# Kernel tuning notes

Measured on AMD Instinct MI355X. Metric: run time of the kernel, lower is better.

## Reference

```python
import jax, jax.numpy as jnp
import numpy as np
from jax import lax


def _mdlstm_dir(x, Wx, Wh, Wv, b):
    # x: [H, W, B, Cin]; one diagonal-causal 2D-LSTM scan (top-left origin).
    H, W, B, Cin = x.shape
    C = Wh.shape[0]
    xa = jnp.einsum('hwbi,ic->hwbc', x, Wx) + b  # [H,W,B,5C] precomputed input gates

    def col_step(carry, inp):
        h_l, c_l = carry                    # left neighbor [B,C]
        xa_ij, h_u, c_u = inp               # input preact, up neighbor
        a = xa_ij + h_l @ Wh + h_u @ Wv     # [B,5C]
        i, f1, f2, o, g = jnp.split(a, 5, axis=-1)
        c = jax.nn.sigmoid(i) * jnp.tanh(g) + jax.nn.sigmoid(f1) * c_l + jax.nn.sigmoid(f2) * c_u
        h = jax.nn.sigmoid(o) * jnp.tanh(c)
        return (h, c), (h, c)

    z = jnp.zeros((B, C), x.dtype)
    zrow = jnp.zeros((W, B, C), x.dtype)

    def row_step(carry, xa_row):
        h_up, c_up = carry                  # [W,B,C]
        _, (hs, cs) = lax.scan(col_step, (z, z), (xa_row, h_up, c_up))
        return (hs, cs), hs

    _, hh = lax.scan(row_step, (zrow, zrow), xa)  # [H,W,B,C]
    return hh


def _mdlstm4(x, Wx, Wh, Wv, b):
    # x: [B,Cin,H,W] -> per-direction outputs [4,H,W,B,C] (directions: TL, TR, BL, BR origins)
    xt = jnp.transpose(x, (2, 3, 0, 1))  # [H,W,B,Cin]
    x4 = jnp.stack([xt, xt[:, ::-1], xt[::-1], xt[::-1, ::-1]])
    o = jax.vmap(_mdlstm_dir)(x4, Wx, Wh, Wv, b)  # [4,H,W,B,C]
    return jnp.stack([o[0], o[1][:, ::-1], o[2][::-1], o[3][::-1, ::-1]])


def _block(x, Wx, Wh, Wv, b, cw, cb):
    h4 = _mdlstm4(x, Wx, Wh, Wv, b)            # [4,H,W,B,C]
    h = jnp.transpose(h4.sum(0), (2, 3, 0, 1))  # sum directions -> [B,C,H,W]
    y = lax.conv_general_dilated(h, cw, window_strides=(2, 2), padding='VALID',
                                 dimension_numbers=('NCHW', 'OIHW', 'NCHW'))
    return jnp.tanh(y + cb[None, :, None, None])


def _forward(x, p0_Wx, p0_Wh, p0_Wv, p0_b, c0_w, c0_b,
             p1_Wx, p1_Wh, p1_Wv, p1_b, c1_w, c1_b,
             p2_Wx, p2_Wh, p2_Wv, p2_b, dW, db):
    x = _block(x, p0_Wx, p0_Wh, p0_Wv, p0_b, c0_w, c0_b)  # [B,6,31,126]
    x = _block(x, p1_Wx, p1_Wh, p1_Wv, p1_b, c1_w, c1_b)  # [B,20,14,61]
    h4 = _mdlstm4(x, p2_Wx, p2_Wh, p2_Wv, p2_b)           # [4,H,W,B,50]
    # per-direction Linear(50->100) then sum over the 4 directions
    out = jnp.einsum('dhwbc,dcn->bhwn', h4, dW) + db.sum(0)
    return out  # [B,14,61,100]


def setup_inputs() -> dict:
    key = jax.random.key(0)
    ks = jax.random.split(key, 20)
    rn = lambda k, s, sc=0.1: jax.random.normal(k, s, jnp.float32) * sc
    return {
        'x': jax.random.normal(ks[0], (16, 1, 64, 256), jnp.float32),
        'p0_Wx': rn(ks[1], (4, 1, 10)), 'p0_Wh': rn(ks[2], (4, 2, 10)),
        'p0_Wv': rn(ks[3], (4, 2, 10)), 'p0_b': rn(ks[4], (4, 10)),
        'c0_w': rn(ks[5], (6, 2, 2, 4)), 'c0_b': rn(ks[6], (6,)),
        'p1_Wx': rn(ks[7], (4, 6, 50)), 'p1_Wh': rn(ks[8], (4, 10, 50)),
        'p1_Wv': rn(ks[9], (4, 10, 50)), 'p1_b': rn(ks[10], (4, 50)),
        'c1_w': rn(ks[11], (20, 10, 2, 4)), 'c1_b': rn(ks[12], (20,)),
        'p2_Wx': rn(ks[13], (4, 20, 250)), 'p2_Wh': rn(ks[14], (4, 50, 250)),
        'p2_Wv': rn(ks[15], (4, 50, 250)), 'p2_b': rn(ks[16], (4, 250)),
        'dW': rn(ks[17], (4, 50, 100)), 'db': rn(ks[18], (4, 100)),
    }


def reference(x, p0_Wx, p0_Wh, p0_Wv, p0_b, c0_w, c0_b,
              p1_Wx, p1_Wh, p1_Wv, p1_b, c1_w, c1_b,
              p2_Wx, p2_Wh, p2_Wv, p2_b, dW, db):
    return _forward(x, p0_Wx, p0_Wh, p0_Wv, p0_b, c0_w, c0_b,
                    p1_Wx, p1_Wh, p1_Wv, p1_b, c1_w, c1_b,
                    p2_Wx, p2_Wh, p2_Wv, p2_b, dW, db)
```

## Files before the change

### kernel.cpp

```cpp
#include <hip/hip_runtime.h>

typedef unsigned short ushort_t;
typedef __attribute__((ext_vector_type(8))) short short8;
typedef __attribute__((ext_vector_type(4))) float float4_t;
typedef __attribute__((ext_vector_type(2))) float v2f;

__device__ __forceinline__ float frcp(float x) { return __builtin_amdgcn_rcpf(x); }
__device__ __forceinline__ float fsig(float x) { return frcp(1.f + __expf(-x)); }
__device__ __forceinline__ float ftanh(float x) { return 1.f - 2.f * frcp(1.f + __expf(2.f * x)); }
__device__ __forceinline__ float sig_e2(float a) { return frcp(1.f + __builtin_amdgcn_exp2f(a)); }
__device__ __forceinline__ float th_e2(float a) { return 1.f - 2.f * frcp(1.f + __builtin_amdgcn_exp2f(a)); }

__device__ __forceinline__ ushort_t f2bf(float f) {
    union { float f; unsigned u; } v; v.f = f;
    unsigned u = v.u;
    unsigned r = (u + 0x7fffu + ((u >> 16) & 1u)) >> 16;
    return (ushort_t)r;
}
__device__ __forceinline__ float bf2f(ushort_t s) {
    union { unsigned u; float f; } v; v.u = ((unsigned)s) << 16;
    return v.f;
}
__device__ __forceinline__ float dpp_shr1(float x) {
    int i = __builtin_bit_cast(int, x);
    int r = __builtin_amdgcn_update_dpp(0, i, 0x138 , 0xf, 0xf, true);
    return __builtin_bit_cast(float, r);
}

__global__ __launch_bounds__(64) void k_mdlstm0(
    const float* __restrict__ x, const float* __restrict__ Wx,
    const float* __restrict__ Wh, const float* __restrict__ Wv,
    const float* __restrict__ bias, float* __restrict__ h0)
{
    const int dir = blockIdx.x >> 4, b = blockIdx.x & 15;
    const int lane = threadIdx.x;
    const bool fH = dir >= 2, fW = (dir & 1) != 0;
    const int ri = fH ? 63 - lane : lane;
    const float L2E = 1.44269504088896340736f;

    __shared__ float Xs[64 * 256];
    {
        const float* xg = x + b * 64 * 256;
        for (int i4 = lane; i4 < 4096; i4 += 64) {
            int row = i4 >> 6, c4 = (i4 & 63) << 2;
            float4 v = *(const float4*)(xg + (row << 8) + c4);
            *(float4*)&Xs[(row << 8) + c4] = v;
        }
    }
    __syncthreads();

    v2f wx[5], bs[5], wh0[5], wh1[5], wv0[5], wv1[5];
#pragma unroll
    for (int g = 0; g < 5; g++) {
        float sc = (g == 4) ? 2.f * L2E : -L2E;
#pragma unroll
        for (int un = 0; un < 2; un++) {
            int n = g * 2 + un;
            wx[g][un]  = Wx[dir * 10 + n] * sc;
            bs[g][un]  = bias[dir * 10 + n] * sc;
            wh0[g][un] = Wh[(dir * 2 + 0) * 10 + n] * sc;
            wh1[g][un] = Wh[(dir * 2 + 1) * 10 + n] * sc;
            wv0[g][un] = Wv[(dir * 2 + 0) * 10 + n] * sc;
            wv1[g][un] = Wv[(dir * 2 + 1) * 10 + n] * sc;
        }
    }

    float* orow = h0 + (((dir * 16 + b) * 64 + ri) * 256) * 2;
    v2f hr = {0.f, 0.f}, cr = {0.f, 0.f};

    auto ld = [&](int d) -> float {
        int j = d - lane; j = j < 0 ? 0 : (j > 255 ? 255 : j);
        int cj = fW ? 255 - j : j;
        return Xs[(ri << 8) + cj];
    };
    float xp0 = ld(0), xp1 = ld(1);

    for (int d = 0; d < 319; d++) {
        float xv = xp0;
        xp0 = xp1;
        xp1 = ld(d + 2);

        float hu0 = dpp_shr1(hr.x), hu1 = dpp_shr1(hr.y);
        float cu0 = dpp_shr1(cr.x), cu1 = dpp_shr1(cr.y);

        int j = d - lane;
        if (j >= 0 && j < 256) {
            v2f a[5];
#pragma unroll
            for (int g = 0; g < 5; g++) {
                v2f t = __builtin_elementwise_fma((v2f){xv, xv}, wx[g], bs[g]);
                t = __builtin_elementwise_fma((v2f){hr.x, hr.x}, wh0[g], t);
                t = __builtin_elementwise_fma((v2f){hr.y, hr.y}, wh1[g], t);
                t = __builtin_elementwise_fma((v2f){hu0, hu0}, wv0[g], t);
                t = __builtin_elementwise_fma((v2f){hu1, hu1}, wv1[g], t);
                a[g] = t;
            }
            v2f si  = {sig_e2(a[0].x), sig_e2(a[0].y)};
            v2f sf1 = {sig_e2(a[1].x), sig_e2(a[1].y)};
            v2f sf2 = {sig_e2(a[2].x), sig_e2(a[2].y)};
            v2f so  = {sig_e2(a[3].x), sig_e2(a[3].y)};
            v2f tg  = {th_e2(a[4].x),  th_e2(a[4].y)};
            v2f cu  = {cu0, cu1};
            v2f cn = si * tg + sf1 * cr + sf2 * cu;
            v2f tc = {th_e2(cn.x * (2.f * L2E)), th_e2(cn.y * (2.f * L2E))};
            hr = so * tc;
            cr = cn;
            int cj = fW ? 255 - j : j;
            float2 hv; hv.x = hr.x; hv.y = hr.y;
            *(float2*)&orow[cj * 2] = hv;
        } else {
            hr = (v2f){0.f, 0.f};
            cr = (v2f){0.f, 0.f};
        }
    }
}

__global__ __launch_bounds__(128) void k_conv0(
    const float* __restrict__ h0, const float* __restrict__ cw,
    const float* __restrict__ cb, float* __restrict__ x1)
{
    int blk = blockIdx.x;
    int oh = blk / 127, ow = blk % 127;
    int t = threadIdx.x;
    if (t >= 96) return;
    int b = t / 6, co = t % 6;
    float w[2][2][4];
#pragma unroll
    for (int ci = 0; ci < 2; ci++)
#pragma unroll
        for (int kh = 0; kh < 2; kh++)
#pragma unroll
            for (int kw = 0; kw < 4; kw++)
                w[ci][kh][kw] = cw[((co * 2 + ci) * 2 + kh) * 4 + kw];
    float acc = cb[co];
    for (int dirb = 0; dirb < 4; dirb++) {
#pragma unroll
        for (int kh = 0; kh < 2; kh++) {
#pragma unroll
            for (int kw = 0; kw < 4; kw++) {
                const float* ptr = h0 + ((((dirb * 16 + b) * 64) + (2 * oh + kh)) * 256 + (2 * ow + kw)) * 2;
                float2 hv = *(const float2*)ptr;
                acc = fmaf(hv.x, w[0][kh][kw], acc);
                acc = fmaf(hv.y, w[1][kh][kw], acc);
            }
        }
    }
    x1[((oh * 127 + ow) * 16 + b) * 6 + co] = ftanh(acc);
}

__global__ __launch_bounds__(1024, 1) void k_mdlstm1(
    const float* __restrict__ x1, const float* __restrict__ Wx,
    const float* __restrict__ Wh, const float* __restrict__ Wv,
    const float* __restrict__ bias, float* __restrict__ h1)
{
    const int dir = blockIdx.x >> 4, b = blockIdx.x & 15;
    const bool fH = dir >= 2, fW = (dir & 1) != 0;
    const int tid = threadIdx.x;
    const int wave = tid >> 6, lane = tid & 63;

    __shared__ float Xs1[32 * 127 * 6];
    __shared__ __align__(16) ushort_t Ah[2][32][40];
    __shared__ __align__(16) ushort_t Al[2][32][40];
    __shared__ float P[32][68];
    __shared__ float cbuf[2][33][12];

    for (int i = tid; i < 2 * 32 * 40; i += 1024) { ((ushort_t*)Ah)[i] = 0; ((ushort_t*)Al)[i] = 0; }
    for (int i = tid; i < 2 * 33 * 12; i += 1024) ((float*)cbuf)[i] = 0.f;
    for (int i = tid; i < 32 * 127 * 6; i += 1024)
        Xs1[i] = x1[(i / 6) * 96 + b * 6 + (i % 6)];
    __syncthreads();
    if (tid < 6) {
        int rr = fH ? 31 : 0, cc = fW ? 126 : 0;
        float xv = Xs1[(rr * 127 + cc) * 6 + tid];
        ushort_t xh = f2bf(xv);
        Ah[0][0][20 + tid] = xh;
        Al[0][0][20 + tid] = f2bf(xv - bf2f(xh));
    }

    const int mt = wave & 1, nt = wave >> 1;
    short8 bh = {0,0,0,0,0,0,0,0}, bl = {0,0,0,0,0,0,0,0};
    if (wave < 8) {
        int n = nt * 16 + (lane & 15);
#pragma unroll
        for (int jj = 0; jj < 8; jj++) {
            int k = (lane >> 4) * 8 + jj;
            float v = 0.f;
            if (n < 50) {
                if (k < 10)      v = Wh[(dir * 10 + k) * 50 + n];
                else if (k < 20) v = Wv[(dir * 10 + (k - 10)) * 50 + n];
                else if (k < 26) v = Wx[(dir * 6 + (k - 20)) * 50 + n];
            }
            ushort_t hi = f2bf(v);
            bh[jj] = (short)hi;
            bl[jj] = (short)f2bf(v - bf2f(hi));
        }
    }

    const int cell = tid / 10, u = tid % 10;
    float br[5];
#pragma unroll
    for (int g = 0; g < 5; g++) br[g] = (tid < 320) ? bias[dir * 50 + g * 10 + u] : 0.f;
    const int ri = fH ? 31 - cell : cell;
    float creg = 0.f;
    __syncthreads();

    int p = 0;
    for (int d = 0; d < 158; d++) {
        if (wave < 8) {
            const int arow = mt * 16 + (lane & 15);
            const int koff = (lane >> 4) * 8;
            short8 ah = *(const short8*)&Ah[p][arow][koff];
            short8 al = *(const short8*)&Al[p][arow][koff];
            float4_t acc = {0.f, 0.f, 0.f, 0.f};
            acc = __builtin_amdgcn_mfma_f32_16x16x32_bf16(ah, bh, acc, 0, 0, 0);
            acc = __builtin_amdgcn_mfma_f32_16x16x32_bf16(al, bh, acc, 0, 0, 0);
            acc = __builtin_amdgcn_mfma_f32_16x16x32_bf16(ah, bl, acc, 0, 0, 0);
            int col = nt * 16 + (lane & 15);
            int r0 = (lane >> 4) * 4;
#pragma unroll
            for (int r = 0; r < 4; r++) P[mt * 16 + r0 + r][col] = acc[r];
        } else if (tid >= 512 && tid < 704) {
            int s = tid - 512, xc = s / 6, ci = s % 6;
            int jn = d + 1 - xc;
            if (jn >= 0 && jn < 127) {
                int rr = fH ? 31 - xc : xc, cc = fW ? 126 - jn : jn;
                float xv = Xs1[(rr * 127 + cc) * 6 + ci];
                ushort_t xh = f2bf(xv);
                Ah[1 - p][xc][20 + ci] = xh;
                Al[1 - p][xc][20 + ci] = f2bf(xv - bf2f(xh));
            }
        }
        __syncthreads();

        if (tid < 320) {
            int j = d - cell;
            if (j >= 0 && j < 127) {
                float ai  = P[cell][u]      + br[0];
                float af1 = P[cell][10 + u] + br[1];
                float af2 = P[cell][20 + u] + br[2];
                float ao  = P[cell][30 + u] + br[3];
                float ag  = P[cell][40 + u] + br[4];
                float cu = cbuf[p][cell][u];
                float cn = fsig(ai) * ftanh(ag) + fsig(af1) * creg + fsig(af2) * cu;
                float hn = fsig(ao) * ftanh(cn);
                creg = cn;
                cbuf[1 - p][cell + 1][u] = cn;
                ushort_t hh = f2bf(hn);
                float hhf = bf2f(hh);
                ushort_t hlo = f2bf(hn - hhf);
                Ah[1 - p][cell][u] = hh;
                Al[1 - p][cell][u] = hlo;
                if (cell < 31) { Ah[1 - p][cell + 1][10 + u] = hh; Al[1 - p][cell + 1][10 + u] = hlo; }
                int cj = fW ? 126 - j : j;
                h1[(((dir * 16 + b) * 32 + ri) * 127 + cj) * 10 + u] = hn;
            }
        }
        __syncthreads();
        p ^= 1;
    }
}

__global__ __launch_bounds__(320, 1) void k_conv1(
    const float* __restrict__ h1, const float* __restrict__ cw,
    const float* __restrict__ cb, float* __restrict__ x2)
{
    int blk = blockIdx.x;
    int oh = blk / 62, ow = blk % 62;
    int t = threadIdx.x;
    int b = t / 20, co = t % 20;
    float w[10][2][4];
#pragma unroll
    for (int ci = 0; ci < 10; ci++)
#pragma unroll
        for (int kh = 0; kh < 2; kh++)
#pragma unroll
            for (int kw = 0; kw < 4; kw++)
                w[ci][kh][kw] = cw[((co * 10 + ci) * 2 + kh) * 4 + kw];
    float acc = cb[co];
    for (int dirb = 0; dirb < 4; dirb++) {
#pragma unroll
        for (int kh = 0; kh < 2; kh++) {
#pragma unroll
            for (int kw = 0; kw < 4; kw++) {
                const float* ptr = h1 + ((((dirb * 16 + b) * 32) + (2 * oh + kh)) * 127 + (2 * ow + kw)) * 10;
#pragma unroll
                for (int ci = 0; ci < 10; ci++)
                    acc = fmaf(ptr[ci], w[ci][kh][kw], acc);
            }
        }
    }
    x2[((oh * 62 + ow) * 16 + b) * 20 + co] = ftanh(acc);
}

__global__ __launch_bounds__(256) void k_prepB2(
    const float* __restrict__ Wh, const float* __restrict__ Wv,
    const float* __restrict__ Wx, ushort_t* __restrict__ Bh,
    ushort_t* __restrict__ Bl)
{
    int idx = blockIdx.x * 256 + threadIdx.x;
    if (idx >= 131072) return;
    int dir = idx >> 15; int k = (idx >> 8) & 127; int n = idx & 255;
    float v = 0.f;
    if (n < 250) {
        if (k < 50)       v = Wh[(dir * 50 + k) * 250 + n];
        else if (k < 100) v = Wv[(dir * 50 + (k - 50)) * 250 + n];
        else if (k < 120) v = Wx[(dir * 20 + (k - 100)) * 250 + n];
    }
    ushort_t hi = f2bf(v);
    Bh[idx] = hi;
    Bl[idx] = f2bf(v - bf2f(hi));
}

__global__ __launch_bounds__(1024, 1) void k_mdlstm2(
    const float* __restrict__ x2, const ushort_t* __restrict__ BmH,
    const ushort_t* __restrict__ BmL,
    const float* __restrict__ bias, float* __restrict__ h2)
{
    const int dir = blockIdx.x >> 4, b = blockIdx.x & 15;
    const bool fH = dir >= 2, fW = (dir & 1) != 0;
    const int tid = threadIdx.x;
    const int wave = tid >> 6, lane = tid & 63;

    __shared__ float Xs2[16 * 62 * 20];
    __shared__ __align__(16) ushort_t Ah[2][16][136];
    __shared__ __align__(16) ushort_t Al[2][16][136];
    __shared__ float P[16][260];
    __shared__ float cbuf[2][16][52];

    for (int i = tid; i < 2 * 16 * 136; i += 1024) { ((ushort_t*)Ah)[i] = 0; ((ushort_t*)Al)[i] = 0; }
    for (int i = tid; i < 16 * 62 * 20; i += 1024)
        Xs2[i] = x2[(i / 20) * 320 + b * 20 + (i % 20)];
    __syncthreads();
    if (tid < 20) {
        int ci = tid;
        int rr = fH ? 15 : 0, cc = fW ? 61 : 0;
        float xv = Xs2[(rr * 62 + cc) * 20 + ci];
        ushort_t xh = f2bf(xv);
        Ah[0][0][100 + ci] = xh;
        Al[0][0][100 + ci] = f2bf(xv - bf2f(xh));
    }

    short8 bfragH[4], bfragL[4];
    {
        const int n = wave * 16 + (lane & 15);
#pragma unroll
        for (int q = 0; q < 4; q++) {
#pragma unroll
            for (int jj = 0; jj < 8; jj++) {
                int k = q * 32 + (lane >> 4) * 8 + jj;
                bfragH[q][jj] = (short)BmH[(dir * 128 + k) * 256 + n];
                bfragL[q][jj] = (short)BmL[(dir * 128 + k) * 256 + n];
            }
        }
    }

    const int cell = tid / 50, u = tid % 50;
    float bi = 0, bf1 = 0, bf2v = 0, bo = 0, bg = 0;
    if (tid < 800) {
        bi   = bias[dir * 250 + u];
        bf1  = bias[dir * 250 + 50 + u];
        bf2v = bias[dir * 250 + 100 + u];
        bo   = bias[dir * 250 + 150 + u];
        bg   = bias[dir * 250 + 200 + u];
    }
    const int rr_c = fH ? 15 - cell : cell;
    float creg = 0.f;
    __syncthreads();

    int p = 0;
    for (int d = 0; d < 77; d++) {
        {
            const int arow = lane & 15;
            const int koff = (lane >> 4) * 8;
            short8 ah[4], al[4];
#pragma unroll
            for (int q = 0; q < 4; q++) {
                ah[q] = *(const short8*)&Ah[p][arow][q * 32 + koff];
                al[q] = *(const short8*)&Al[p][arow][q * 32 + koff];
            }
            float4_t acc = {0.f, 0.f, 0.f, 0.f};
#pragma unroll
            for (int q = 0; q < 4; q++) acc = __builtin_amdgcn_mfma_f32_16x16x32_bf16(ah[q], bfragH[q], acc, 0, 0, 0);
#pragma unroll
            for (int q = 0; q < 4; q++) acc = __builtin_amdgcn_mfma_f32_16x16x32_bf16(al[q], bfragH[q], acc, 0, 0, 0);
#pragma unroll
            for (int q = 0; q < 4; q++) acc = __builtin_amdgcn_mfma_f32_16x16x32_bf16(ah[q], bfragL[q], acc, 0, 0, 0);
            int col = wave * 16 + (lane & 15);
            int r0 = (lane >> 4) * 4;
#pragma unroll
            for (int r = 0; r < 4; r++) P[r0 + r][col] = acc[r];
        }
        __syncthreads();

        if (tid < 800) {
            int j = d - cell;
            if (j >= 0 && j < 62) {
                float ai  = P[cell][u] + bi;
                float af1 = P[cell][50 + u] + bf1;
                float af2 = P[cell][100 + u] + bf2v;
                float ao  = P[cell][150 + u] + bo;
                float ag  = P[cell][200 + u] + bg;
                float cu = (cell == 0) ? 0.f : cbuf[p][cell - 1][u];
                float cn = fsig(ai) * ftanh(ag) + fsig(af1) * creg + fsig(af2) * cu;
                float hn = fsig(ao) * ftanh(cn);
                creg = cn;
                cbuf[1 - p][cell][u] = cn;
                ushort_t hh = f2bf(hn);
                float hhf = bf2f(hh);
                ushort_t hlo = f2bf(hn - hhf);
                Ah[1 - p][cell][u] = hh;
                Al[1 - p][cell][u] = hlo;
                if (cell < 15) { Ah[1 - p][cell + 1][50 + u] = hh; Al[1 - p][cell + 1][50 + u] = hlo; }
                int cc = fW ? 61 - j : j;
                h2[(((dir * 16 + b) * 16 + rr_c) * 62 + cc) * 50 + u] = hn;
            }
        } else if (tid >= 832 && tid < 992) {
            int s = tid - 832;
#pragma unroll
            for (int it = 0; it < 2; it++) {
                int item = s + it * 160;
                int xc = item / 20, ci = item % 20;
                int jn = d + 1 - xc;
                if (jn >= 0 && jn < 62) {
                    int rr = fH ? 15 - xc : xc, cc = fW ? 61 - jn : jn;
                    float xv = Xs2[(rr * 62 + cc) * 20 + ci];
                    ushort_t xh = f2bf(xv);
                    Ah[1 - p][xc][100 + ci] = xh;
                    Al[1 - p][xc][100 + ci] = f2bf(xv - bf2f(xh));
                }
            }
        }
        __syncthreads();
        p ^= 1;
    }
}

__global__ __launch_bounds__(256) void k_final(
    const float* __restrict__ h2, const float* __restrict__ dW,
    const float* __restrict__ db, float* __restrict__ out)
{
    int blk = blockIdx.x;
    int r = blk / 62, c = blk % 62;
    int t = threadIdx.x;
    __shared__ float hb[3200];
    for (int i = t; i < 3200; i += 256) {
        int dirb = i / 800, rem = i % 800, b = rem / 50, u = rem % 50;
        hb[i] = h2[(((dirb * 16 + b) * 16 + r) * 62 + c) * 50 + u];
    }
    __syncthreads();
    for (int o = t; o < 1600; o += 256) {
        int b = o / 100, n = o % 100;
        float acc = db[n] + db[100 + n] + db[200 + n] + db[300 + n];
#pragma unroll
        for (int dirb = 0; dirb < 4; dirb++) {
            const float* hp = hb + (dirb * 16 + b) * 50;
            const float* wp = dW + dirb * 5000 + n;
#pragma unroll 10
            for (int cc2 = 0; cc2 < 50; cc2++)
                acc = fmaf(hp[cc2], wp[cc2 * 100], acc);
        }
        out[((b * 16 + r) * 62 + c) * 100 + n] = acc;
    }
}

extern "C" void kernel_launch(void* const* d_in, const int* in_sizes, int n_in,
                              void* d_out, int out_size, void* d_ws, size_t ws_size,
                              hipStream_t stream)
{
    const float* x     = (const float*)d_in[0];
    const float* p0_Wx = (const float*)d_in[1];
    const float* p0_Wh = (const float*)d_in[2];
    const float* p0_Wv = (const float*)d_in[3];
    const float* p0_b  = (const float*)d_in[4];
    const float* c0_w  = (const float*)d_in[5];
    const float* c0_b  = (const float*)d_in[6];
    const float* p1_Wx = (const float*)d_in[7];
    const float* p1_Wh = (const float*)d_in[8];
    const float* p1_Wv = (const float*)d_in[9];
    const float* p1_b  = (const float*)d_in[10];
    const float* c1_w  = (const float*)d_in[11];
    const float* c1_b  = (const float*)d_in[12];
    const float* p2_Wx = (const float*)d_in[13];
    const float* p2_Wh = (const float*)d_in[14];
    const float* p2_Wv = (const float*)d_in[15];
    const float* p2_b  = (const float*)d_in[16];
    const float* dW    = (const float*)d_in[17];
    const float* db    = (const float*)d_in[18];
    float* out = (float*)d_out;
    float* ws  = (float*)d_ws;

    float* h0 = ws;
    float* x1 = h0 + 2097152;
    float* h1 = x1 + 390144;
    float* x2 = h1 + 2600960;
    float* h2 = x2 + 317440;
    ushort_t* BmH = (ushort_t*)(h2 + 3174400);
    ushort_t* BmL = BmH + 131072;

    k_prepB2<<<512, 256, 0, stream>>>(p2_Wh, p2_Wv, p2_Wx, BmH, BmL);
    k_mdlstm0<<<64, 64, 0, stream>>>(x, p0_Wx, p0_Wh, p0_Wv, p0_b, h0);
    k_conv0<<<32 * 127, 128, 0, stream>>>(h0, c0_w, c0_b, x1);
    k_mdlstm1<<<64, 1024, 0, stream>>>(x1, p1_Wx, p1_Wh, p1_Wv, p1_b, h1);
    k_conv1<<<16 * 62, 320, 0, stream>>>(h1, c1_w, c1_b, x2);
    k_mdlstm2<<<64, 1024, 0, stream>>>(x2, BmH, BmL, p2_b, h2);
    k_final<<<16 * 62, 256, 0, stream>>>(h2, dW, db, out);
}
```

Before: 477.3 us.

## Interleave gates per unit in layer-2 MFMA tiles and fuse LSTM update; unroll layer-0 diagonal

```diff
diff --git a/kernel.cpp b/kernel.cpp
--- a/kernel.cpp
+++ b/kernel.cpp
@@ -66,51 +66,69 @@
     }
 
     float* orow = h0 + (((dir * 16 + b) * 64 + ri) * 256) * 2;
-    v2f hr = {0.f, 0.f}, cr = {0.f, 0.f};
-
-    auto ld = [&](int d) -> float {
-        int j = d - lane; j = j < 0 ? 0 : (j > 255 ? 255 : j);
-        int cj = fW ? 255 - j : j;
+    v2f hB = {0.f, 0.f}, cB = {0.f, 0.f};
+
+    auto ldx = [&](int j) -> float {
+        int jc = j < 0 ? 0 : (j > 255 ? 255 : j);
+        int cj = fW ? 255 - jc : jc;
         return Xs[(ri << 8) + cj];
     };
-    float xp0 = ld(0), xp1 = ld(1);
-
-    for (int d = 0; d < 319; d++) {
-        float xv = xp0;
-        xp0 = xp1;
-        xp1 = ld(d + 2);
-
-        float hu0 = dpp_shr1(hr.x), hu1 = dpp_shr1(hr.y);
-        float cu0 = dpp_shr1(cr.x), cu1 = dpp_shr1(cr.y);
-
-        int j = d - lane;
-        if (j >= 0 && j < 256) {
-            v2f a[5];
-#pragma unroll
-            for (int g = 0; g < 5; g++) {
-                v2f t = __builtin_elementwise_fma((v2f){xv, xv}, wx[g], bs[g]);
-                t = __builtin_elementwise_fma((v2f){hr.x, hr.x}, wh0[g], t);
-                t = __builtin_elementwise_fma((v2f){hr.y, hr.y}, wh1[g], t);
-                t = __builtin_elementwise_fma((v2f){hu0, hu0}, wv0[g], t);
-                t = __builtin_elementwise_fma((v2f){hu1, hu1}, wv1[g], t);
-                a[g] = t;
-            }
-            v2f si  = {sig_e2(a[0].x), sig_e2(a[0].y)};
-            v2f sf1 = {sig_e2(a[1].x), sig_e2(a[1].y)};
-            v2f sf2 = {sig_e2(a[2].x), sig_e2(a[2].y)};
-            v2f so  = {sig_e2(a[3].x), sig_e2(a[3].y)};
-            v2f tg  = {th_e2(a[4].x),  th_e2(a[4].y)};
-            v2f cu  = {cu0, cu1};
-            v2f cn = si * tg + sf1 * cr + sf2 * cu;
-            v2f tc = {th_e2(cn.x * (2.f * L2E)), th_e2(cn.y * (2.f * L2E))};
-            hr = so * tc;
-            cr = cn;
-            int cj = fW ? 255 - j : j;
-            float2 hv; hv.x = hr.x; hv.y = hr.y;
+    auto cellf = [&](float xv, v2f hl, v2f cl, float hu0, float hu1,
+                     float cu0, float cu1, v2f& hn, v2f& cn) {
+        v2f a[5];
+#pragma unroll
+        for (int g = 0; g < 5; g++) {
+            v2f t = __builtin_elementwise_fma((v2f){xv, xv}, wx[g], bs[g]);
+            t = __builtin_elementwise_fma((v2f){hl.x, hl.x}, wh0[g], t);
+            t = __builtin_elementwise_fma((v2f){hl.y, hl.y}, wh1[g], t);
+            t = __builtin_elementwise_fma((v2f){hu0, hu0}, wv0[g], t);
+            t = __builtin_elementwise_fma((v2f){hu1, hu1}, wv1[g], t);
+            a[g] = t;
+        }
+        v2f si  = {sig_e2(a[0].x), sig_e2(a[0].y)};
+        v2f sf1 = {sig_e2(a[1].x), sig_e2(a[1].y)};
+        v2f sf2 = {sig_e2(a[2].x), sig_e2(a[2].y)};
+        v2f so  = {sig_e2(a[3].x), sig_e2(a[3].y)};
+        v2f tg  = {th_e2(a[4].x),  th_e2(a[4].y)};
+        v2f cu  = {cu0, cu1};
+        cn = si * tg + sf1 * cl + sf2 * cu;
+        v2f tc = {th_e2(cn.x * (2.f * L2E)), th_e2(cn.y * (2.f * L2E))};
+        hn = so * tc;
+    };
+
+    float xA0 = ldx(0 - lane), xB0 = ldx(1 - lane);
+    float xA1 = ldx(2 - lane), xB1 = ldx(3 - lane);
+
+    for (int t = 0; t < 160; t++) {
+        const int jA = 2 * t - lane, jB = jA + 1;
+        float xA = xA0, xB = xB0;
+        xA0 = xA1; xB0 = xB1;
+        xA1 = ldx(2 * (t + 2) - lane); xB1 = ldx(2 * (t + 2) + 1 - lane);
+
+        float huA0 = dpp_shr1(hB.x), huA1 = dpp_shr1(hB.y);
+        float cuA0 = dpp_shr1(cB.x), cuA1 = dpp_shr1(cB.y);
+        v2f hA, cA;
+        cellf(xA, hB, cB, huA0, huA1, cuA0, cuA1, hA, cA);
+        bool actA = (jA >= 0) && (jA < 256);
+        if (!actA) { hA = (v2f){0.f, 0.f}; cA = (v2f){0.f, 0.f}; }
+
+        float huB0 = dpp_shr1(hA.x), huB1 = dpp_shr1(hA.y);
+        float cuB0 = dpp_shr1(cA.x), cuB1 = dpp_shr1(cA.y);
+        v2f hN, cN;
+        cellf(xB, hA, cA, huB0, huB1, cuB0, cuB1, hN, cN);
+        bool actB = (jB >= 0) && (jB < 256);
+        if (!actB) { hN = (v2f){0.f, 0.f}; cN = (v2f){0.f, 0.f}; }
+        hB = hN; cB = cN;
+
+        if (actA) {
+            int cj = fW ? 255 - jA : jA;
+            float2 hv; hv.x = hA.x; hv.y = hA.y;
             *(float2*)&orow[cj * 2] = hv;
-        } else {
-            hr = (v2f){0.f, 0.f};
-            cr = (v2f){0.f, 0.f};
+        }
+        if (actB) {
+            int cj = fW ? 255 - jB : jB;
+            float2 hv; hv.x = hB.x; hv.y = hB.y;
+            *(float2*)&orow[cj * 2] = hv;
         }
     }
 }
@@ -298,10 +316,15 @@
     ushort_t* __restrict__ Bl)
 {
     int idx = blockIdx.x * 256 + threadIdx.x;
-    if (idx >= 131072) return;
-    int dir = idx >> 15; int k = (idx >> 8) & 127; int n = idx & 255;
+    if (idx >= 262144) return;
+    int jj = idx & 7, lane = (idx >> 3) & 63, q = (idx >> 9) & 3;
+    int nt = (idx >> 11) & 31, dir = idx >> 16;
+    int k = q * 32 + (lane >> 4) * 8 + jj;
+    int col = nt * 16 + (lane & 15);
+    int unit = col >> 3, gate = col & 7;
     float v = 0.f;
-    if (n < 250) {
+    if (unit < 50 && gate < 5) {
+        int n = gate * 50 + unit;
         if (k < 50)       v = Wh[(dir * 50 + k) * 250 + n];
         else if (k < 100) v = Wv[(dir * 50 + (k - 50)) * 250 + n];
         else if (k < 120) v = Wx[(dir * 20 + (k - 100)) * 250 + n];
@@ -312,121 +335,131 @@
 }
 
 __global__ __launch_bounds__(1024, 1) void k_mdlstm2(
-    const float* __restrict__ x2, const ushort_t* __restrict__ BmH,
-    const ushort_t* __restrict__ BmL,
+    const float* __restrict__ x2, const ushort_t* __restrict__ BfH,
+    const ushort_t* __restrict__ BfL,
     const float* __restrict__ bias, float* __restrict__ h2)
 {
     const int dir = blockIdx.x >> 4, b = blockIdx.x & 15;
     const bool fH = dir >= 2, fW = (dir & 1) != 0;
     const int tid = threadIdx.x;
     const int wave = tid >> 6, lane = tid & 63;
+    const int quad = lane >> 4, g_self = lane & 7, uloc = (lane >> 3) & 1;
+    const float L2E = 1.44269504088896340736f;
 
     __shared__ float Xs2[16 * 62 * 20];
     __shared__ __align__(16) ushort_t Ah[2][16][136];
     __shared__ __align__(16) ushort_t Al[2][16][136];
-    __shared__ float P[16][260];
-    __shared__ float cbuf[2][16][52];
 
     for (int i = tid; i < 2 * 16 * 136; i += 1024) { ((ushort_t*)Ah)[i] = 0; ((ushort_t*)Al)[i] = 0; }
     for (int i = tid; i < 16 * 62 * 20; i += 1024)
         Xs2[i] = x2[(i / 20) * 320 + b * 20 + (i % 20)];
     __syncthreads();
     if (tid < 20) {
-        int ci = tid;
         int rr = fH ? 15 : 0, cc = fW ? 61 : 0;
-        float xv = Xs2[(rr * 62 + cc) * 20 + ci];
+        float xv = Xs2[(rr * 62 + cc) * 20 + tid];
         ushort_t xh = f2bf(xv);
-        Ah[0][0][100 + ci] = xh;
-        Al[0][0][100 + ci] = f2bf(xv - bf2f(xh));
-    }
-
-    short8 bfragH[4], bfragL[4];
-    {
-        const int n = wave * 16 + (lane & 15);
-#pragma unroll
-        for (int q = 0; q < 4; q++) {
-#pragma unroll
-            for (int jj = 0; jj < 8; jj++) {
-                int k = q * 32 + (lane >> 4) * 8 + jj;
-                bfragH[q][jj] = (short)BmH[(dir * 128 + k) * 256 + n];
-                bfragL[q][jj] = (short)BmL[(dir * 128 + k) * 256 + n];
-            }
-        }
-    }
-
-    const int cell = tid / 50, u = tid % 50;
-    float bi = 0, bf1 = 0, bf2v = 0, bo = 0, bg = 0;
-    if (tid < 800) {
-        bi   = bias[dir * 250 + u];
-        bf1  = bias[dir * 250 + 50 + u];
-        bf2v = bias[dir * 250 + 100 + u];
-        bo   = bias[dir * 250 + 150 + u];
-        bg   = bias[dir * 250 + 200 + u];
-    }
-    const int rr_c = fH ? 15 - cell : cell;
-    float creg = 0.f;
+        Ah[0][0][100 + tid] = xh;
+        Al[0][0][100 + tid] = f2bf(xv - bf2f(xh));
+    }
+
+    const bool mwave = wave < 13;
+    const float s_c = (g_self == 4) ? 2.f * L2E : -L2E;
+    const float a_c = (g_self == 4) ? -2.f : 1.f;
+    const float c_c = (g_self == 4) ? 1.f : 0.f;
+
+    int unitr[2];
+    float biasr[2];
+#pragma unroll
+    for (int t = 0; t < 2; t++) {
+        int nt = 2 * wave + t;
+        int un = 2 * nt + uloc;
+        unitr[t] = un;
+        biasr[t] = (mwave && un < 50 && g_self < 5) ? bias[dir * 250 + g_self * 50 + un] : 0.f;
+    }
+    const ushort_t* pBh = BfH + (size_t)(dir * 32 + 2 * wave) * 2048 + lane * 8;
+    const ushort_t* pBl = BfL + (size_t)(dir * 32 + 2 * wave) * 2048 + lane * 8;
+
+    float cprev[2][4] = {{0.f, 0.f, 0.f, 0.f}, {0.f, 0.f, 0.f, 0.f}};
     __syncthreads();
 
     int p = 0;
     for (int d = 0; d < 77; d++) {
-        {
+        if (mwave) {
+            float4_t acc0 = {0.f, 0.f, 0.f, 0.f}, acc1 = {0.f, 0.f, 0.f, 0.f};
             const int arow = lane & 15;
             const int koff = (lane >> 4) * 8;
-            short8 ah[4], al[4];
 #pragma unroll
             for (int q = 0; q < 4; q++) {
-                ah[q] = *(const short8*)&Ah[p][arow][q * 32 + koff];
-                al[q] = *(const short8*)&Al[p][arow][q * 32 + koff];
-            }
-            float4_t acc = {0.f, 0.f, 0.f, 0.f};
-#pragma unroll
-            for (int q = 0; q < 4; q++) acc = __builtin_amdgcn_mfma_f32_16x16x32_bf16(ah[q], bfragH[q], acc, 0, 0, 0);
-#pragma unroll
-            for (int q = 0; q < 4; q++) acc = __builtin_amdgcn_mfma_f32_16x16x32_bf16(al[q], bfragH[q], acc, 0, 0, 0);
-#pragma unroll
-            for (int q = 0; q < 4; q++) acc = __builtin_amdgcn_mfma_f32_16x16x32_bf16(ah[q], bfragL[q], acc, 0, 0, 0);
-            int col = wave * 16 + (lane & 15);
-            int r0 = (lane >> 4) * 4;
-#pragma unroll
-            for (int r = 0; r < 4; r++) P[r0 + r][col] = acc[r];
-        }
-        __syncthreads();
-
-        if (tid < 800) {
-            int j = d - cell;
-            if (j >= 0 && j < 62) {
-                float ai  = P[cell][u] + bi;
-                float af1 = P[cell][50 + u] + bf1;
-                float af2 = P[cell][100 + u] + bf2v;
-                float ao  = P[cell][150 + u] + bo;
-                float ag  = P[cell][200 + u] + bg;
-                float cu = (cell == 0) ? 0.f : cbuf[p][cell - 1][u];
-                float cn = fsig(ai) * ftanh(ag) + fsig(af1) * creg + fsig(af2) * cu;
-                float hn = fsig(ao) * ftanh(cn);
-                creg = cn;
-                cbuf[1 - p][cell][u] = cn;
-                ushort_t hh = f2bf(hn);
-                float hhf = bf2f(hh);
-                ushort_t hlo = f2bf(hn - hhf);
-                Ah[1 - p][cell][u] = hh;
-                Al[1 - p][cell][u] = hlo;
-                if (cell < 15) { Ah[1 - p][cell + 1][50 + u] = hh; Al[1 - p][cell + 1][50 + u] = hlo; }
-                int cc = fW ? 61 - j : j;
-                h2[(((dir * 16 + b) * 16 + rr_c) * 62 + cc) * 50 + u] = hn;
-            }
-        } else if (tid >= 832 && tid < 992) {
+                short8 b0h = *(const short8*)(pBh + q * 512);
+                short8 b0l = *(const short8*)(pBl + q * 512);
+                short8 b1h = *(const short8*)(pBh + 2048 + q * 512);
+                short8 b1l = *(const short8*)(pBl + 2048 + q * 512);
+                short8 ah = *(const short8*)&Ah[p][arow][q * 32 + koff];
+                short8 al = *(const short8*)&Al[p][arow][q * 32 + koff];
+                acc0 = __builtin_amdgcn_mfma_f32_16x16x32_bf16(ah, b0h, acc0, 0, 0, 0);
+                acc0 = __builtin_amdgcn_mfma_f32_16x16x32_bf16(al, b0h, acc0, 0, 0, 0);
+                acc0 = __builtin_amdgcn_mfma_f32_16x16x32_bf16(ah, b0l, acc0, 0, 0, 0);
+                acc1 = __builtin_amdgcn_mfma_f32_16x16x32_bf16(ah, b1h, acc1, 0, 0, 0);
+                acc1 = __builtin_amdgcn_mfma_f32_16x16x32_bf16(al, b1h, acc1, 0, 0, 0);
+                acc1 = __builtin_amdgcn_mfma_f32_16x16x32_bf16(ah, b1l, acc1, 0, 0, 0);
+            }
+            const int gbase = lane & ~7;
+#pragma unroll
+            for (int t = 0; t < 2; t++) {
+                float4_t acc = t ? acc1 : acc0;
+                float nl[4];
+#pragma unroll
+                for (int r = 0; r < 4; r++) {
+                    float pre = acc[r] + biasr[t];
+                    nl[r] = c_c + a_c * frcp(1.f + __builtin_amdgcn_exp2f(s_c * pre));
+                }
+                float cold[4];
+#pragma unroll
+                for (int r = 0; r < 4; r++) cold[r] = cprev[t][r];
+                float cup = __shfl_up(cold[3], 16);
+#pragma unroll
+                for (int r = 0; r < 4; r++) {
+                    float pi  = __shfl(nl[r], gbase + 0);
+                    float pf1 = __shfl(nl[r], gbase + 1);
+                    float pf2 = __shfl(nl[r], gbase + 2);
+                    float po  = __shfl(nl[r], gbase + 3);
+                    float pg  = __shfl(nl[r], gbase + 4);
+                    int cell = quad * 4 + r;
+                    int j = d - cell;
+                    bool active = (j >= 0) && (j < 62);
+                    float cu = (r == 0) ? (quad ? cup : 0.f) : cold[r - 1];
+                    float cn = pi * pg + pf1 * cold[r] + pf2 * cu;
+                    cn = active ? cn : cold[r];
+                    cprev[t][r] = cn;
+                    float hn = po * (1.f - 2.f * frcp(1.f + __builtin_amdgcn_exp2f(2.f * L2E * cn)));
+                    if (g_self == 0 && unitr[t] < 50 && active) {
+                        int u = unitr[t];
+                        ushort_t hh = f2bf(hn);
+                        float hhf = bf2f(hh);
+                        ushort_t hlo = f2bf(hn - hhf);
+                        Ah[1 - p][cell][u] = hh;
+                        Al[1 - p][cell][u] = hlo;
+                        if (cell < 15) { Ah[1 - p][cell + 1][50 + u] = hh; Al[1 - p][cell + 1][50 + u] = hlo; }
+                        int rr = fH ? 15 - cell : cell, cc = fW ? 61 - j : j;
+                        h2[(((dir * 16 + b) * 16 + rr) * 62 + cc) * 50 + u] = hn;
+                    }
+                }
+            }
+        } else {
             int s = tid - 832;
 #pragma unroll
             for (int it = 0; it < 2; it++) {
-                int item = s + it * 160;
-                int xc = item / 20, ci = item % 20;
-                int jn = d + 1 - xc;
-                if (jn >= 0 && jn < 62) {
-                    int rr = fH ? 15 - xc : xc, cc = fW ? 61 - jn : jn;
-                    float xv = Xs2[(rr * 62 + cc) * 20 + ci];
-                    ushort_t xh = f2bf(xv);
-                    Ah[1 - p][xc][100 + ci] = xh;
-                    Al[1 - p][xc][100 + ci] = f2bf(xv - bf2f(xh));
+                int item = s + it * 192;
+                if (item < 320) {
+                    int xc = item / 20, ci = item % 20;
+                    int jn = d + 1 - xc;
+                    if (jn >= 0 && jn < 62) {
+                        int rr = fH ? 15 - xc : xc, cc = fW ? 61 - jn : jn;
+                        float xv = Xs2[(rr * 62 + cc) * 20 + ci];
+                        ushort_t xh = f2bf(xv);
+                        Ah[1 - p][xc][100 + ci] = xh;
+                        Al[1 - p][xc][100 + ci] = f2bf(xv - bf2f(xh));
+                    }
                 }
             }
         }
@@ -494,14 +527,14 @@
     float* h1 = x1 + 390144;
     float* x2 = h1 + 2600960;
     float* h2 = x2 + 317440;
-    ushort_t* BmH = (ushort_t*)(h2 + 3174400);
-    ushort_t* BmL = BmH + 131072;
-
-    k_prepB2<<<512, 256, 0, stream>>>(p2_Wh, p2_Wv, p2_Wx, BmH, BmL);
+    ushort_t* BfH = (ushort_t*)(h2 + 3174400);
+    ushort_t* BfL = BfH + 262144;
+
+    k_prepB2<<<1024, 256, 0, stream>>>(p2_Wh, p2_Wv, p2_Wx, BfH, BfL);
     k_mdlstm0<<<64, 64, 0, stream>>>(x, p0_Wx, p0_Wh, p0_Wv, p0_b, h0);
     k_conv0<<<32 * 127, 128, 0, stream>>>(h0, c0_w, c0_b, x1);
     k_mdlstm1<<<64, 1024, 0, stream>>>(x1, p1_Wx, p1_Wh, p1_Wv, p1_b, h1);
     k_conv1<<<16 * 62, 320, 0, stream>>>(h1, c1_w, c1_b, x2);
-    k_mdlstm2<<<64, 1024, 0, stream>>>(x2, BmH, BmL, p2_b, h2);
+    k_mdlstm2<<<64, 1024, 0, stream>>>(x2, BfH, BfL, p2_b, h2);
     k_final<<<16 * 62, 256, 0, stream>>>(h2, dW, db, out);
 }
```

After: 661.3 us. 1.39x slower.

## Replace transcendental builtins with FMA polynomial exp2/rcp and unroll diagonal loop by two

Applied to the files above, without the earlier changes.

```diff
diff --git a/kernel.cpp b/kernel.cpp
--- a/kernel.cpp
+++ b/kernel.cpp
@@ -10,6 +10,30 @@
 __device__ __forceinline__ float ftanh(float x) { return 1.f - 2.f * frcp(1.f + __expf(2.f * x)); }
 __device__ __forceinline__ float sig_e2(float a) { return frcp(1.f + __builtin_amdgcn_exp2f(a)); }
 __device__ __forceinline__ float th_e2(float a) { return 1.f - 2.f * frcp(1.f + __builtin_amdgcn_exp2f(a)); }
+
+__device__ __forceinline__ float exp2_fma(float a) {
+    a = fminf(fmaxf(a, -60.f), 60.f);
+    float k = floorf(a);
+    float f = a - k;
+    float p = fmaf(f, 1.54035304e-4f, 1.33335581e-3f);
+    p = fmaf(f, p, 9.61812911e-3f);
+    p = fmaf(f, p, 5.55041087e-2f);
+    p = fmaf(f, p, 2.40226507e-1f);
+    p = fmaf(f, p, 6.93147181e-1f);
+    p = fmaf(f, p, 1.0f);
+    int ik = (int)k;
+    float sc = __builtin_bit_cast(float, (ik + 127) << 23);
+    return p * sc;
+}
+__device__ __forceinline__ float rcp_fma(float y) {
+    int i = 0x7EF311C3 - __builtin_bit_cast(int, y);
+    float r = __builtin_bit_cast(float, i);
+    r = r * fmaf(-y, r, 2.0f);
+    r = r * fmaf(-y, r, 2.0f);
+    return r;
+}
+__device__ __forceinline__ float sig_e2f(float a) { return rcp_fma(1.f + exp2_fma(a)); }
+__device__ __forceinline__ float th_e2f(float a)  { return fmaf(-2.f, rcp_fma(1.f + exp2_fma(a)), 1.f); }
 
 __device__ __forceinline__ ushort_t f2bf(float f) {
     union { float f; unsigned u; } v; v.f = f;
@@ -66,51 +90,69 @@
     }
 
     float* orow = h0 + (((dir * 16 + b) * 64 + ri) * 256) * 2;
-    v2f hr = {0.f, 0.f}, cr = {0.f, 0.f};
-
-    auto ld = [&](int d) -> float {
-        int j = d - lane; j = j < 0 ? 0 : (j > 255 ? 255 : j);
-        int cj = fW ? 255 - j : j;
+    v2f hB = {0.f, 0.f}, cB = {0.f, 0.f};
+
+    auto ldx = [&](int j) -> float {
+        int jc = j < 0 ? 0 : (j > 255 ? 255 : j);
+        int cj = fW ? 255 - jc : jc;
         return Xs[(ri << 8) + cj];
     };
-    float xp0 = ld(0), xp1 = ld(1);
-
-    for (int d = 0; d < 319; d++) {
-        float xv = xp0;
-        xp0 = xp1;
-        xp1 = ld(d + 2);
-
-        float hu0 = dpp_shr1(hr.x), hu1 = dpp_shr1(hr.y);
-        float cu0 = dpp_shr1(cr.x), cu1 = dpp_shr1(cr.y);
-
-        int j = d - lane;
-        if (j >= 0 && j < 256) {
-            v2f a[5];
-#pragma unroll
-            for (int g = 0; g < 5; g++) {
-                v2f t = __builtin_elementwise_fma((v2f){xv, xv}, wx[g], bs[g]);
-                t = __builtin_elementwise_fma((v2f){hr.x, hr.x}, wh0[g], t);
-                t = __builtin_elementwise_fma((v2f){hr.y, hr.y}, wh1[g], t);
-                t = __builtin_elementwise_fma((v2f){hu0, hu0}, wv0[g], t);
-                t = __builtin_elementwise_fma((v2f){hu1, hu1}, wv1[g], t);
-                a[g] = t;
-            }
-            v2f si  = {sig_e2(a[0].x), sig_e2(a[0].y)};
-            v2f sf1 = {sig_e2(a[1].x), sig_e2(a[1].y)};
-            v2f sf2 = {sig_e2(a[2].x), sig_e2(a[2].y)};
-            v2f so  = {sig_e2(a[3].x), sig_e2(a[3].y)};
-            v2f tg  = {th_e2(a[4].x),  th_e2(a[4].y)};
-            v2f cu  = {cu0, cu1};
-            v2f cn = si * tg + sf1 * cr + sf2 * cu;
-            v2f tc = {th_e2(cn.x * (2.f * L2E)), th_e2(cn.y * (2.f * L2E))};
-            hr = so * tc;
-            cr = cn;
-            int cj = fW ? 255 - j : j;
-            float2 hv; hv.x = hr.x; hv.y = hr.y;
+    auto cellf = [&](float xv, v2f hl, v2f cl, float hu0, float hu1,
+                     float cu0, float cu1, v2f& hn, v2f& cn) {
+        v2f a[5];
+#pragma unroll
+        for (int g = 0; g < 5; g++) {
+            v2f t = __builtin_elementwise_fma((v2f){xv, xv}, wx[g], bs[g]);
+            t = __builtin_elementwise_fma((v2f){hl.x, hl.x}, wh0[g], t);
+            t = __builtin_elementwise_fma((v2f){hl.y, hl.y}, wh1[g], t);
+            t = __builtin_elementwise_fma((v2f){hu0, hu0}, wv0[g], t);
+            t = __builtin_elementwise_fma((v2f){hu1, hu1}, wv1[g], t);
+            a[g] = t;
+        }
+        v2f si  = {sig_e2f(a[0].x), sig_e2f(a[0].y)};
+        v2f sf1 = {sig_e2f(a[1].x), sig_e2f(a[1].y)};
+        v2f sf2 = {sig_e2f(a[2].x), sig_e2f(a[2].y)};
+        v2f so  = {sig_e2f(a[3].x), sig_e2f(a[3].y)};
+        v2f tg  = {th_e2f(a[4].x),  th_e2f(a[4].y)};
+        v2f cu  = {cu0, cu1};
+        cn = si * tg + sf1 * cl + sf2 * cu;
+        v2f tc = {th_e2f(cn.x * (2.f * L2E)), th_e2f(cn.y * (2.f * L2E))};
+        hn = so * tc;
+    };
+
+    float xA0 = ldx(0 - lane), xB0 = ldx(1 - lane);
+    float xA1 = ldx(2 - lane), xB1 = ldx(3 - lane);
+
+    for (int t = 0; t < 160; t++) {
+        const int jA = 2 * t - lane, jB = jA + 1;
+        float xA = xA0, xB = xB0;
+        xA0 = xA1; xB0 = xB1;
+        xA1 = ldx(2 * (t + 2) - lane); xB1 = ldx(2 * (t + 2) + 1 - lane);
+
+        float huA0 = dpp_shr1(hB.x), huA1 = dpp_shr1(hB.y);
+        float cuA0 = dpp_shr1(cB.x), cuA1 = dpp_shr1(cB.y);
+        v2f hA, cA;
+        cellf(xA, hB, cB, huA0, huA1, cuA0, cuA1, hA, cA);
+        bool actA = (jA >= 0) && (jA < 256);
+        if (!actA) { hA = (v2f){0.f, 0.f}; cA = (v2f){0.f, 0.f}; }
+
+        float huB0 = dpp_shr1(hA.x), huB1 = dpp_shr1(hA.y);
+        float cuB0 = dpp_shr1(cA.x), cuB1 = dpp_shr1(cA.y);
+        v2f hN, cN;
+        cellf(xB, hA, cA, huB0, huB1, cuB0, cuB1, hN, cN);
+        bool actB = (jB >= 0) && (jB < 256);
+        if (!actB) { hN = (v2f){0.f, 0.f}; cN = (v2f){0.f, 0.f}; }
+        hB = hN; cB = cN;
+
+        if (actA) {
+            int cj = fW ? 255 - jA : jA;
+            float2 hv; hv.x = hA.x; hv.y = hA.y;
             *(float2*)&orow[cj * 2] = hv;
-        } else {
-            hr = (v2f){0.f, 0.f};
-            cr = (v2f){0.f, 0.f};
+        }
+        if (actB) {
+            int cj = fW ? 255 - jB : jB;
+            float2 hv; hv.x = hB.x; hv.y = hB.y;
+            *(float2*)&orow[cj * 2] = hv;
         }
     }
 }
```

New measurement: 538.4 us. 12.8% more time.
